# Optimization experiments

Measured on AMD Instinct MI355X. Metric: run time of the kernel, lower is better.

The kernel has to match this reference:

```python
import jax, jax.numpy as jnp
import numpy as np

N_NODES = 50000
N_EDGES = 800000
IN_F, HID_F, OUT_F = 256, 128, 64


def setup_inputs() -> dict:
    key = jax.random.key(0)
    ks = jax.random.split(key, 9)
    glorot = lambda k, shp: jax.random.normal(k, shp, jnp.float32) * np.sqrt(2.0 / (shp[0] + shp[1]))
    return {
        "x": jax.random.normal(ks[0], (N_NODES, IN_F), jnp.float32),
        "W1": glorot(ks[1], (IN_F, HID_F)),
        "b1": jnp.zeros((HID_F,), jnp.float32),
        "W2": glorot(ks[2], (HID_F, OUT_F)),
        "b2": jnp.zeros((OUT_F,), jnp.float32),
        "Wf": glorot(ks[3], (OUT_F, 2)),
        "bf": jnp.zeros((2,), jnp.float32),
        "src": jax.random.randint(ks[4], (N_EDGES,), 0, N_NODES, jnp.int32),
        "dst": jax.random.randint(ks[5], (N_EDGES,), 0, N_NODES, jnp.int32),
    }


def _gcn_layer(x, src, dst, W, b):
    # DGL GraphConv, norm='both': h = D_in^{-1/2} A D_out^{-1/2} (x W) + b
    n = x.shape[0]
    ones = jnp.ones((src.shape[0],), x.dtype)
    deg_out = jnp.clip(jax.ops.segment_sum(ones, src, num_segments=n), 1.0)
    deg_in = jnp.clip(jax.ops.segment_sum(ones, dst, num_segments=n), 1.0)
    h = x @ W  # transform first (in_feats >= out_feats), cheaper messages
    h = h * jax.lax.rsqrt(deg_out)[:, None]
    agg = jax.ops.segment_sum(h[src], dst, num_segments=n)  # [N, F] sparse aggregate
    return agg * jax.lax.rsqrt(deg_in)[:, None] + b


def reference(x, W1, b1, W2, b2, Wf, bf, src, dst):
    h1 = jax.nn.relu(_gcn_layer(x, src, dst, W1, b1))
    hidden = _gcn_layer(h1, src, dst, W2, b2)
    logits = hidden @ Wf + bf
    return (logits, hidden)
```

## Files before the change

### kernel.cpp

```cpp
#include <hip/hip_runtime.h>
#include <hip/hip_bf16.h>
#include <cstdint>
#include <cstddef>

#define NNODES 50000
#define NEDGES 800000
#define DHB    64
#define DHC    12500
#define NCH    256
#define CHUNK1 3125
#define NBUCK  196

typedef unsigned short u16;
typedef unsigned int u32;
typedef short bfrag8 __attribute__((ext_vector_type(8)));
typedef float f32x4 __attribute__((ext_vector_type(4)));

__device__ __forceinline__ u16 f2bf(float f) {
    union { float f; uint32_t i; } v; v.f = f;
    uint32_t r = (v.i + 0x7FFFu + ((v.i >> 16) & 1u)) >> 16;
    return (u16)r;
}
__device__ __forceinline__ float bflo(u32 p) { union { uint32_t i; float f; } v; v.i = p << 16; return v.f; }
__device__ __forceinline__ float bfhi(u32 p) { union { uint32_t i; float f; } v; v.i = p & 0xFFFF0000u; return v.f; }

__global__ __launch_bounds__(256) void pre_kernel(const float* __restrict__ W1, const float* __restrict__ W2,
                                                  u16* __restrict__ P1, u16* __restrict__ P2,
                                                  const int* __restrict__ src, const int* __restrict__ dst,
                                                  u32* __restrict__ histg, u32* __restrict__ gh1, int nE) {
    __shared__ u32 hh[NNODES / 2];
    int b = blockIdx.x, t = threadIdx.x;
    if (b < DHB) {
        for (int j = t; j < NNODES / 2; j += 256) hh[j] = 0;
        __syncthreads();
        int beg = b * DHC, end = min(beg + DHC, nE);
        for (int i = beg + t; i < end; i += 256) {
            u32 n = (u32)src[i];
            atomicAdd(&hh[n >> 1], 1u << ((n & 1) * 16));
        }
        __syncthreads();
        u32* out = histg + (size_t)b * (NNODES / 2);
        for (int j = t; j < NNODES / 2; j += 256) out[j] = hh[j];
    } else if (b < DHB + NCH) {
        int c = b - DHB;
        hh[t] = 0;
        __syncthreads();
        int beg = c * CHUNK1, end = min(beg + CHUNK1, nE);
        for (int i = beg + t; i < end; i += 256)
            atomicAdd(&hh[(u32)dst[i] >> 8], 1);
        __syncthreads();
        gh1[t * NCH + c] = hh[t];
    } else {
        int i = (b - DHB - NCH) * 256 + t;
        if (i < 256 * 128) {
            int k = i >> 7, n = i & 127;
            P1[((((k >> 3) << 7) + n) << 3) | (k & 7)] = f2bf(W1[i]);
        }
        if (i < 128 * 64) {
            int k = i >> 6, n = i & 63;
            P2[((((k >> 3) << 6) + n) << 3) | (k & 7)] = f2bf(W2[i]);
        }
    }
}

__global__ __launch_bounds__(256) void red_scan1(const u32* __restrict__ histg, int* __restrict__ deg,
                                                 const u32* __restrict__ gh1, int* __restrict__ scan1,
                                                 int* __restrict__ part1) {
    int t = threadIdx.x, b = blockIdx.x;
    int n = b * 196 + t;
    if (t < 196 && n < NNODES) {
        int s = 0;
        #pragma unroll 4
        for (int bb = 0; bb < DHB; bb++)
            s += (int)((histg[(size_t)bb * (NNODES / 2) + (n >> 1)] >> ((n & 1) * 16)) & 0xFFFFu);
        deg[n] = s;
    }
    __shared__ int sd[256];
    int gi = b * NCH + t;
    int v = (int)gh1[gi];
    sd[t] = v;
    __syncthreads();
    #pragma unroll
    for (int o = 1; o < 256; o <<= 1) {
        int add = (t >= o) ? sd[t - o] : 0;
        __syncthreads();
        sd[t] += add;
        __syncthreads();
    }
    scan1[gi] = sd[t];
    if (t == 255) part1[b] = sd[255];
}

__global__ __launch_bounds__(256) void scatter1(const int* __restrict__ dst, const int* __restrict__ src,
                                                const u32* __restrict__ gh1, const int* __restrict__ scan1,
                                                const int* __restrict__ part1, u32* __restrict__ sbuf, int nE) {
    __shared__ int sd[256];
    __shared__ int offs[256];
    __shared__ u32 base[256];
    __shared__ u32 lh[256];
    int t = threadIdx.x, c = blockIdx.x;
    int v = part1[t];
    sd[t] = v;
    __syncthreads();
    #pragma unroll
    for (int o = 1; o < 256; o <<= 1) {
        int add = (t >= o) ? sd[t - o] : 0;
        __syncthreads();
        sd[t] += add;
        __syncthreads();
    }
    offs[t] = sd[t] - v;
    __syncthreads();
    base[t] = (u32)(scan1[t * NCH + c] + offs[t] - (int)gh1[t * NCH + c]);
    lh[t] = 0;
    __syncthreads();
    int beg = c * CHUNK1, end = min(beg + CHUNK1, nE);
    for (int i = beg + t; i < end; i += 256) {
        u32 el = ((u32)dst[i] << 16) | (u32)src[i];
        u32 d = el >> 24;
        u32 r = atomicAdd(&lh[d], 1);
        sbuf[base[d] + r] = el;
    }
}

__global__ __launch_bounds__(256) void sort_bucket(const u32* __restrict__ sbuf, const int* __restrict__ part1,
                                                   u32* __restrict__ sorted, int* __restrict__ rp, int nE) {
    __shared__ int sd[256];
    __shared__ int cnt[256];
    __shared__ int cursor[256];
    int t = threadIdx.x, b = blockIdx.x;
    int v = part1[t];
    sd[t] = v;
    __syncthreads();
    #pragma unroll
    for (int o = 1; o < 256; o <<= 1) {
        int add = (t >= o) ? sd[t - o] : 0;
        __syncthreads();
        sd[t] += add;
        __syncthreads();
    }
    __shared__ int bs_s, bl_s;
    if (t == b) { bs_s = sd[t] - v; bl_s = v; }
    __syncthreads();
    int bstart = bs_s, bend = bstart + bl_s;
    cnt[t] = 0;
    __syncthreads();
    for (int i = bstart + t; i < bend; i += 256)
        atomicAdd(&cnt[(sbuf[i] >> 16) & 255u], 1);
    __syncthreads();
    int cv = cnt[t];
    sd[t] = cv;
    __syncthreads();
    #pragma unroll
    for (int o = 1; o < 256; o <<= 1) {
        int add = (t >= o) ? sd[t - o] : 0;
        __syncthreads();
        sd[t] += add;
        __syncthreads();
    }
    int excl = sd[t] - cv;
    int node = b * 256 + t;
    if (node < NNODES) rp[node] = bstart + excl;
    if (b == NBUCK - 1 && t == 0) rp[NNODES] = nE;
    cursor[t] = excl;
    __syncthreads();
    for (int i = bstart + t; i < bend; i += 256) {
        u32 el = sbuf[i];
        int r = atomicAdd(&cursor[(el >> 16) & 255u], 1);
        sorted[bstart + r] = el;
    }
}


template <int K, int N, bool AF32>
__global__ __launch_bounds__(256) void gemm_scaled(const void* __restrict__ A_, const u16* __restrict__ Wp,
                                                   const int* __restrict__ deg, u16* __restrict__ out, int M) {
    const int lane = threadIdx.x & 63;
    const int wave = threadIdx.x >> 6;
    const int m = lane & 15;
    const int q = lane >> 4;
    const int row0 = blockIdx.x * 64 + wave * 16;

    int rowa = row0 + m; if (rowa > M - 1) rowa = M - 1;

    constexpr int NT = N / 16;
    f32x4 acc[NT];
    #pragma unroll
    for (int t = 0; t < NT; t++) acc[t] = (f32x4){0.f, 0.f, 0.f, 0.f};

    #pragma unroll
    for (int kc = 0; kc < K; kc += 32) {
        bfrag8 af;
        if constexpr (AF32) {
            const float* ap = (const float*)A_ + (size_t)rowa * K + q * 8 + kc;
            const float4 x0 = *(const float4*)(ap);
            const float4 x1 = *(const float4*)(ap + 4);
            af[0] = (short)f2bf(x0.x); af[1] = (short)f2bf(x0.y);
            af[2] = (short)f2bf(x0.z); af[3] = (short)f2bf(x0.w);
            af[4] = (short)f2bf(x1.x); af[5] = (short)f2bf(x1.y);
            af[6] = (short)f2bf(x1.z); af[7] = (short)f2bf(x1.w);
        } else {
            const u16* ap = (const u16*)A_ + (size_t)rowa * K + q * 8 + kc;
            af = *(const bfrag8*)ap;
        }
        const u16* bbase = Wp + ((size_t)(((kc >> 3) + q) * N) + m) * 8;
        #pragma unroll
        for (int t = 0; t < NT; t++) {
            bfrag8 bf_ = *(const bfrag8*)(bbase + t * 128);
            acc[t] = __builtin_amdgcn_mfma_f32_16x16x32_bf16(af, bf_, acc[t], 0, 0, 0);
        }
    }
    #pragma unroll
    for (int r = 0; r < 4; r++) {
        int gr = row0 + q * 4 + r;
        if (gr < M) {
            int dO = deg[gr]; if (dO < 1) dO = 1;
            float s = rsqrtf((float)dO);
            #pragma unroll
            for (int t = 0; t < NT; t++)
                out[(size_t)gr * N + t * 16 + m] = f2bf(acc[t][r] * s);
        }
    }
}

__global__ __launch_bounds__(256) void gather1(const uint4* __restrict__ h, const int* __restrict__ row_ptr,
                                               const u32* __restrict__ sorted, const float* __restrict__ b1,
                                               uint4* __restrict__ h1out, int nNodes) {
    int node = (blockIdx.x * 256 + threadIdx.x) >> 4;
    int l = threadIdx.x & 15;
    if (node >= nNodes) return;
    int beg = row_ptr[node], end = row_ptr[node + 1];
    float a[8] = {0.f, 0.f, 0.f, 0.f, 0.f, 0.f, 0.f, 0.f};
    for (int e = beg; e < end; e += 8) {
        uint4 p[8];
        #pragma unroll
        for (int j = 0; j < 8; j++) {
            int ee = e + j; ee = (ee < end - 1) ? ee : end - 1;
            p[j] = h[(size_t)(sorted[ee] & 0xFFFFu) * 16 + l];
        }
        #pragma unroll
        for (int j = 0; j < 8; j++)
            if (e + j < end) {
                a[0] += bflo(p[j].x); a[1] += bfhi(p[j].x);
                a[2] += bflo(p[j].y); a[3] += bfhi(p[j].y);
                a[4] += bflo(p[j].z); a[5] += bfhi(p[j].z);
                a[6] += bflo(p[j].w); a[7] += bfhi(p[j].w);
            }
    }
    int dI = end - beg; if (dI < 1) dI = 1;
    float r = rsqrtf((float)dI);
    const float4 bA = *(const float4*)(b1 + 8 * l);
    const float4 bB = *(const float4*)(b1 + 8 * l + 4);
    float v0 = fmaxf(a[0] * r + bA.x, 0.f), v1 = fmaxf(a[1] * r + bA.y, 0.f);
    float v2 = fmaxf(a[2] * r + bA.z, 0.f), v3 = fmaxf(a[3] * r + bA.w, 0.f);
    float v4 = fmaxf(a[4] * r + bB.x, 0.f), v5 = fmaxf(a[5] * r + bB.y, 0.f);
    float v6 = fmaxf(a[6] * r + bB.z, 0.f), v7 = fmaxf(a[7] * r + bB.w, 0.f);
    uint4 o;
    o.x = ((u32)f2bf(v1) << 16) | f2bf(v0);
    o.y = ((u32)f2bf(v3) << 16) | f2bf(v2);
    o.z = ((u32)f2bf(v5) << 16) | f2bf(v4);
    o.w = ((u32)f2bf(v7) << 16) | f2bf(v6);
    h1out[(size_t)node * 16 + l] = o;
}

__global__ __launch_bounds__(256) void gather2(const uint4* __restrict__ h2, const int* __restrict__ row_ptr,
                                               const u32* __restrict__ sorted, const float* __restrict__ b2,
                                               const float* __restrict__ Wf, const float* __restrict__ bfv,
                                               float* __restrict__ logits, float* __restrict__ hidden, int nNodes) {
    int node = (blockIdx.x * 256 + threadIdx.x) >> 3;
    int l = threadIdx.x & 7;
    if (node >= nNodes) return;
    int beg = row_ptr[node], end = row_ptr[node + 1];
    float a[8] = {0.f, 0.f, 0.f, 0.f, 0.f, 0.f, 0.f, 0.f};
    for (int e = beg; e < end; e += 8) {
        uint4 p[8];
        #pragma unroll
        for (int j = 0; j < 8; j++) {
            int ee = e + j; ee = (ee < end - 1) ? ee : end - 1;
            p[j] = h2[(size_t)(sorted[ee] & 0xFFFFu) * 8 + l];
        }
        #pragma unroll
        for (int j = 0; j < 8; j++)
            if (e + j < end) {
                a[0] += bflo(p[j].x); a[1] += bfhi(p[j].x);
                a[2] += bflo(p[j].y); a[3] += bfhi(p[j].y);
                a[4] += bflo(p[j].z); a[5] += bfhi(p[j].z);
                a[6] += bflo(p[j].w); a[7] += bfhi(p[j].w);
            }
    }
    int dI = end - beg; if (dI < 1) dI = 1;
    float r = rsqrtf((float)dI);
    float v[8];
    #pragma unroll
    for (int f = 0; f < 8; f++) v[f] = a[f] * r + b2[8 * l + f];
    float4 oA = {v[0], v[1], v[2], v[3]};
    float4 oB = {v[4], v[5], v[6], v[7]};
    ((float4*)hidden)[(size_t)node * 16 + 2 * l + 0] = oA;
    ((float4*)hidden)[(size_t)node * 16 + 2 * l + 1] = oB;
    float l0 = 0.f, l1 = 0.f;
    #pragma unroll
    for (int f = 0; f < 8; f++) {
        l0 += v[f] * Wf[(8 * l + f) * 2 + 0];
        l1 += v[f] * Wf[(8 * l + f) * 2 + 1];
    }
    #pragma unroll
    for (int off = 4; off > 0; off >>= 1) {
        l0 += __shfl_down(l0, off, 8);
        l1 += __shfl_down(l1, off, 8);
    }
    if (l == 0) {
        logits[(size_t)node * 2 + 0] = l0 + bfv[0];
        logits[(size_t)node * 2 + 1] = l1 + bfv[1];
    }
}

extern "C" void kernel_launch(void* const* d_in, const int* in_sizes, int n_in,
                              void* d_out, int out_size, void* d_ws, size_t ws_size,
                              hipStream_t stream) {
    const float* x   = (const float*)d_in[0];
    const float* W1  = (const float*)d_in[1];
    const float* b1  = (const float*)d_in[2];
    const float* W2  = (const float*)d_in[3];
    const float* b2  = (const float*)d_in[4];
    const float* Wf  = (const float*)d_in[5];
    const float* bfv = (const float*)d_in[6];
    const int* src = (const int*)d_in[7];
    const int* dst = (const int*)d_in[8];

    float* out_logits = (float*)d_out;
    float* out_hidden = (float*)d_out + 2 * NNODES;

    char* ws = (char*)d_ws;
    size_t off = 0;
    auto alloc = [&](size_t bytes) { void* p = ws + off; off += (bytes + 255) & ~(size_t)255; return p; };
    u32*   gh1     = (u32*)alloc(NCH * NCH * 4);
    int*   scan1   = (int*)alloc(NCH * NCH * 4);
    int*   part1   = (int*)alloc(256 * 4);
    u32*   sbuf    = (u32*)alloc((size_t)NEDGES * 4);
    u32*   sorted  = (u32*)alloc((size_t)NEDGES * 4);
    u32*   histg   = (u32*)alloc((size_t)DHB * (NNODES / 2) * 4);
    int*   deg_out = (int*)alloc(NNODES * 4);
    int*   row_ptr = (int*)alloc((NNODES + 1) * 4);
    u16*   Wp1     = (u16*)alloc(256 * 128 * 2);
    u16*   Wp2     = (u16*)alloc(128 * 64 * 2);
    u16*   h       = (u16*)alloc((size_t)NNODES * 128 * 2);
    u16*   h1      = (u16*)alloc((size_t)NNODES * 128 * 2);
    u16*   h2      = (u16*)alloc((size_t)NNODES * 64 * 2);

    pre_kernel<<<DHB + NCH + 128, 256, 0, stream>>>(W1, W2, Wp1, Wp2, src, dst, histg, gh1, NEDGES);
    red_scan1<<<NCH, 256, 0, stream>>>(histg, deg_out, gh1, scan1, part1);
    scatter1<<<NCH, 256, 0, stream>>>(dst, src, gh1, scan1, part1, sbuf, NEDGES);
    sort_bucket<<<NBUCK, 256, 0, stream>>>(sbuf, part1, sorted, row_ptr, NEDGES);
    gemm_scaled<256, 128, true><<<(NNODES + 63) / 64, 256, 0, stream>>>(x, Wp1, deg_out, h, NNODES);
    gather1<<<(NNODES * 16 + 255) / 256, 256, 0, stream>>>((const uint4*)h, row_ptr, sorted, b1,
                                                           (uint4*)h1, NNODES);
    gemm_scaled<128, 64, false><<<(NNODES + 63) / 64, 256, 0, stream>>>(h1, Wp2, deg_out, h2, NNODES);
    gather2<<<(NNODES * 8 + 255) / 256, 256, 0, stream>>>((const uint4*)h2, row_ptr, sorted, b2, Wf, bfv,
                                                          out_logits, out_hidden, NNODES);
}
```

Before: 217.5 us.

## Use global atomic degrees, fuse sort with first GEMM, degree-sort gather nodes

Per-node degrees are now computed with global atomics in the histogram pass, replacing the per-block shared histograms and the reduction kernel. The bucket sort and the first GEMM run in one launch so independent work overlaps. A counting sort of nodes by in-degree (capped at 63) builds a permutation, and both gathers use it so threads in a wave get similar edge counts, reducing divergence. The cost is global atomic contention on the degree arrays, a memset, and scattered output writes through the permutation.

```diff
diff --git a/kernel.cpp b/kernel.cpp
--- a/kernel.cpp
+++ b/kernel.cpp
@@ -5,11 +5,12 @@
 
 #define NNODES 50000
 #define NEDGES 800000
-#define DHB    64
-#define DHC    12500
 #define NCH    256
 #define CHUNK1 3125
 #define NBUCK  196
+#define GB1    782
+#define DPB    64
+#define NPB    782
 
 typedef unsigned short u16;
 typedef unsigned int u32;
@@ -27,31 +28,24 @@
 __global__ __launch_bounds__(256) void pre_kernel(const float* __restrict__ W1, const float* __restrict__ W2,
                                                   u16* __restrict__ P1, u16* __restrict__ P2,
                                                   const int* __restrict__ src, const int* __restrict__ dst,
-                                                  u32* __restrict__ histg, u32* __restrict__ gh1, int nE) {
-    __shared__ u32 hh[NNODES / 2];
+                                                  int* __restrict__ deg_out, int* __restrict__ deg_in,
+                                                  u32* __restrict__ gh1, int nE) {
     int b = blockIdx.x, t = threadIdx.x;
-    if (b < DHB) {
-        for (int j = t; j < NNODES / 2; j += 256) hh[j] = 0;
-        __syncthreads();
-        int beg = b * DHC, end = min(beg + DHC, nE);
+    if (b < NCH) {
+        __shared__ u32 hh[NCH];
+        hh[t] = 0;
+        __syncthreads();
+        int beg = b * CHUNK1, end = min(beg + CHUNK1, nE);
         for (int i = beg + t; i < end; i += 256) {
-            u32 n = (u32)src[i];
-            atomicAdd(&hh[n >> 1], 1u << ((n & 1) * 16));
-        }
-        __syncthreads();
-        u32* out = histg + (size_t)b * (NNODES / 2);
-        for (int j = t; j < NNODES / 2; j += 256) out[j] = hh[j];
-    } else if (b < DHB + NCH) {
-        int c = b - DHB;
-        hh[t] = 0;
-        __syncthreads();
-        int beg = c * CHUNK1, end = min(beg + CHUNK1, nE);
-        for (int i = beg + t; i < end; i += 256)
-            atomicAdd(&hh[(u32)dst[i] >> 8], 1);
-        __syncthreads();
-        gh1[t * NCH + c] = hh[t];
+            int d = dst[i];
+            atomicAdd(&hh[(u32)d >> 8], 1u);
+            atomicAdd(&deg_in[d], 1);
+            atomicAdd(&deg_out[src[i]], 1);
+        }
+        __syncthreads();
+        gh1[t * NCH + b] = hh[t];
     } else {
-        int i = (b - DHB - NCH) * 256 + t;
+        int i = (b - NCH) * 256 + t;
         if (i < 256 * 128) {
             int k = i >> 7, n = i & 127;
             P1[((((k >> 3) << 7) + n) << 3) | (k & 7)] = f2bf(W1[i]);
@@ -63,42 +57,68 @@
     }
 }
 
-__global__ __launch_bounds__(256) void red_scan1(const u32* __restrict__ histg, int* __restrict__ deg,
-                                                 const u32* __restrict__ gh1, int* __restrict__ scan1,
-                                                 int* __restrict__ part1) {
+__global__ __launch_bounds__(256) void scan_hist(const u32* __restrict__ gh1, int* __restrict__ scan1,
+                                                 int* __restrict__ part1, const int* __restrict__ deg_in,
+                                                 int* __restrict__ gdh) {
     int t = threadIdx.x, b = blockIdx.x;
-    int n = b * 196 + t;
-    if (t < 196 && n < NNODES) {
-        int s = 0;
-        #pragma unroll 4
-        for (int bb = 0; bb < DHB; bb++)
-            s += (int)((histg[(size_t)bb * (NNODES / 2) + (n >> 1)] >> ((n & 1) * 16)) & 0xFFFFu);
-        deg[n] = s;
-    }
-    __shared__ int sd[256];
-    int gi = b * NCH + t;
-    int v = (int)gh1[gi];
-    sd[t] = v;
-    __syncthreads();
-    #pragma unroll
-    for (int o = 1; o < 256; o <<= 1) {
-        int add = (t >= o) ? sd[t - o] : 0;
-        __syncthreads();
-        sd[t] += add;
-        __syncthreads();
-    }
-    scan1[gi] = sd[t];
-    if (t == 255) part1[b] = sd[255];
+    if (b < NCH) {
+        __shared__ int sd[256];
+        int gi = b * NCH + t;
+        int v = (int)gh1[gi];
+        sd[t] = v;
+        __syncthreads();
+        #pragma unroll
+        for (int o = 1; o < 256; o <<= 1) {
+            int add = (t >= o) ? sd[t - o] : 0;
+            __syncthreads();
+            sd[t] += add;
+            __syncthreads();
+        }
+        scan1[gi] = sd[t];
+        if (t == 255) part1[b] = sd[255];
+    } else {
+        int pb = b - NCH;
+        __shared__ int cnt[64];
+        if (t < 64) cnt[t] = 0;
+        __syncthreads();
+        int n0 = pb * NPB, n1 = min(n0 + NPB, NNODES);
+        for (int n = n0 + t; n < n1; n += 256) {
+            int d = deg_in[n]; d = d > 63 ? 63 : d;
+            atomicAdd(&cnt[d], 1);
+        }
+        __syncthreads();
+        if (t < 64) gdh[pb * 64 + t] = cnt[t];
+    }
 }
 
 __global__ __launch_bounds__(256) void scatter1(const int* __restrict__ dst, const int* __restrict__ src,
                                                 const u32* __restrict__ gh1, const int* __restrict__ scan1,
-                                                const int* __restrict__ part1, u32* __restrict__ sbuf, int nE) {
+                                                const int* __restrict__ part1, u32* __restrict__ sbuf,
+                                                const int* __restrict__ gdh, int* __restrict__ gbase, int nE) {
+    int t = threadIdx.x, c = blockIdx.x;
+    if (c == NCH) {
+        __shared__ int colsum[64];
+        if (t < 64) {
+            int s = 0;
+            for (int pb = 0; pb < DPB; pb++) s += gdh[pb * 64 + t];
+            colsum[t] = s;
+        }
+        __syncthreads();
+        if (t == 0) {
+            int s = 0;
+            for (int d = 0; d < 64; d++) { int c0 = colsum[d]; colsum[d] = s; s += c0; }
+        }
+        __syncthreads();
+        if (t < 64) {
+            int s = colsum[t];
+            for (int pb = 0; pb < DPB; pb++) { gbase[pb * 64 + t] = s; s += gdh[pb * 64 + t]; }
+        }
+        return;
+    }
     __shared__ int sd[256];
     __shared__ int offs[256];
     __shared__ u32 base[256];
     __shared__ u32 lh[256];
-    int t = threadIdx.x, c = blockIdx.x;
     int v = part1[t];
     sd[t] = v;
     __syncthreads();
@@ -123,63 +143,14 @@
     }
 }
 
-__global__ __launch_bounds__(256) void sort_bucket(const u32* __restrict__ sbuf, const int* __restrict__ part1,
-                                                   u32* __restrict__ sorted, int* __restrict__ rp, int nE) {
-    __shared__ int sd[256];
-    __shared__ int cnt[256];
-    __shared__ int cursor[256];
-    int t = threadIdx.x, b = blockIdx.x;
-    int v = part1[t];
-    sd[t] = v;
-    __syncthreads();
-    #pragma unroll
-    for (int o = 1; o < 256; o <<= 1) {
-        int add = (t >= o) ? sd[t - o] : 0;
-        __syncthreads();
-        sd[t] += add;
-        __syncthreads();
-    }
-    __shared__ int bs_s, bl_s;
-    if (t == b) { bs_s = sd[t] - v; bl_s = v; }
-    __syncthreads();
-    int bstart = bs_s, bend = bstart + bl_s;
-    cnt[t] = 0;
-    __syncthreads();
-    for (int i = bstart + t; i < bend; i += 256)
-        atomicAdd(&cnt[(sbuf[i] >> 16) & 255u], 1);
-    __syncthreads();
-    int cv = cnt[t];
-    sd[t] = cv;
-    __syncthreads();
-    #pragma unroll
-    for (int o = 1; o < 256; o <<= 1) {
-        int add = (t >= o) ? sd[t - o] : 0;
-        __syncthreads();
-        sd[t] += add;
-        __syncthreads();
-    }
-    int excl = sd[t] - cv;
-    int node = b * 256 + t;
-    if (node < NNODES) rp[node] = bstart + excl;
-    if (b == NBUCK - 1 && t == 0) rp[NNODES] = nE;
-    cursor[t] = excl;
-    __syncthreads();
-    for (int i = bstart + t; i < bend; i += 256) {
-        u32 el = sbuf[i];
-        int r = atomicAdd(&cursor[(el >> 16) & 255u], 1);
-        sorted[bstart + r] = el;
-    }
-}
-
-
 template <int K, int N, bool AF32>
-__global__ __launch_bounds__(256) void gemm_scaled(const void* __restrict__ A_, const u16* __restrict__ Wp,
-                                                   const int* __restrict__ deg, u16* __restrict__ out, int M) {
+__device__ __forceinline__ void gemm_body(const void* __restrict__ A_, const u16* __restrict__ Wp,
+                                          const int* __restrict__ deg, u16* __restrict__ out, int M, int bx) {
     const int lane = threadIdx.x & 63;
     const int wave = threadIdx.x >> 6;
     const int m = lane & 15;
     const int q = lane >> 4;
-    const int row0 = blockIdx.x * 64 + wave * 16;
+    const int row0 = bx * 64 + wave * 16;
 
     int rowa = row0 + m; if (rowa > M - 1) rowa = M - 1;
 
@@ -223,12 +194,87 @@
     }
 }
 
+template <int K, int N, bool AF32>
+__global__ __launch_bounds__(256) void gemm_scaled(const void* __restrict__ A_, const u16* __restrict__ Wp,
+                                                   const int* __restrict__ deg, u16* __restrict__ out, int M) {
+    gemm_body<K, N, AF32>(A_, Wp, deg, out, M, blockIdx.x);
+}
+
+__global__ __launch_bounds__(256) void sort_gemm(const u32* __restrict__ sbuf, const int* __restrict__ part1,
+                                                 u32* __restrict__ sorted, int* __restrict__ rp,
+                                                 const float* __restrict__ x, const u16* __restrict__ Wp1,
+                                                 const int* __restrict__ deg_out, const int* __restrict__ deg_in,
+                                                 const int* __restrict__ gbase, int* __restrict__ perm,
+                                                 u16* __restrict__ h, int nE) {
+    int b = blockIdx.x, t = threadIdx.x;
+    if (b < NBUCK) {
+        __shared__ int sd[256];
+        __shared__ int cnt[256];
+        __shared__ int cursor[256];
+        int v = part1[t];
+        sd[t] = v;
+        __syncthreads();
+        #pragma unroll
+        for (int o = 1; o < 256; o <<= 1) {
+            int add = (t >= o) ? sd[t - o] : 0;
+            __syncthreads();
+            sd[t] += add;
+            __syncthreads();
+        }
+        __shared__ int bs_s, bl_s;
+        if (t == b) { bs_s = sd[t] - v; bl_s = v; }
+        __syncthreads();
+        int bstart = bs_s, bend = bstart + bl_s;
+        cnt[t] = 0;
+        __syncthreads();
+        for (int i = bstart + t; i < bend; i += 256)
+            atomicAdd(&cnt[(sbuf[i] >> 16) & 255u], 1);
+        __syncthreads();
+        int cv = cnt[t];
+        sd[t] = cv;
+        __syncthreads();
+        #pragma unroll
+        for (int o = 1; o < 256; o <<= 1) {
+            int add = (t >= o) ? sd[t - o] : 0;
+            __syncthreads();
+            sd[t] += add;
+            __syncthreads();
+        }
+        int excl = sd[t] - cv;
+        int node = b * 256 + t;
+        if (node < NNODES) rp[node] = bstart + excl;
+        if (b == NBUCK - 1 && t == 0) rp[NNODES] = nE;
+        cursor[t] = excl;
+        __syncthreads();
+        for (int i = bstart + t; i < bend; i += 256) {
+            u32 el = sbuf[i];
+            int r = atomicAdd(&cursor[(el >> 16) & 255u], 1);
+            sorted[bstart + r] = el;
+        }
+    } else if (b < NBUCK + GB1) {
+        gemm_body<256, 128, true>(x, Wp1, deg_out, h, NNODES, b - NBUCK);
+    } else {
+        int pb = b - NBUCK - GB1;
+        __shared__ int cur[64];
+        if (t < 64) cur[t] = gbase[pb * 64 + t];
+        __syncthreads();
+        int n0 = pb * NPB, n1 = min(n0 + NPB, NNODES);
+        for (int n = n0 + t; n < n1; n += 256) {
+            int d = deg_in[n]; d = d > 63 ? 63 : d;
+            int p = atomicAdd(&cur[d], 1);
+            perm[p] = n;
+        }
+    }
+}
+
 __global__ __launch_bounds__(256) void gather1(const uint4* __restrict__ h, const int* __restrict__ row_ptr,
                                                const u32* __restrict__ sorted, const float* __restrict__ b1,
+                                               const int* __restrict__ perm,
                                                uint4* __restrict__ h1out, int nNodes) {
-    int node = (blockIdx.x * 256 + threadIdx.x) >> 4;
+    int g = (blockIdx.x * 256 + threadIdx.x) >> 4;
     int l = threadIdx.x & 15;
-    if (node >= nNodes) return;
+    if (g >= nNodes) return;
+    int node = perm[g];
     int beg = row_ptr[node], end = row_ptr[node + 1];
     float a[8] = {0.f, 0.f, 0.f, 0.f, 0.f, 0.f, 0.f, 0.f};
     for (int e = beg; e < end; e += 8) {
@@ -266,10 +312,12 @@
 __global__ __launch_bounds__(256) void gather2(const uint4* __restrict__ h2, const int* __restrict__ row_ptr,
                                                const u32* __restrict__ sorted, const float* __restrict__ b2,
                                                const float* __restrict__ Wf, const float* __restrict__ bfv,
+                                               const int* __restrict__ perm,
                                                float* __restrict__ logits, float* __restrict__ hidden, int nNodes) {
-    int node = (blockIdx.x * 256 + threadIdx.x) >> 3;
+    int g = (blockIdx.x * 256 + threadIdx.x) >> 3;
     int l = threadIdx.x & 7;
-    if (node >= nNodes) return;
+    if (g >= nNodes) return;
+    int node = perm[g];
     int beg = row_ptr[node], end = row_ptr[node + 1];
     float a[8] = {0.f, 0.f, 0.f, 0.f, 0.f, 0.f, 0.f, 0.f};
     for (int e = beg; e < end; e += 8) {
@@ -338,23 +386,29 @@
     int*   part1   = (int*)alloc(256 * 4);
     u32*   sbuf    = (u32*)alloc((size_t)NEDGES * 4);
     u32*   sorted  = (u32*)alloc((size_t)NEDGES * 4);
-    u32*   histg   = (u32*)alloc((size_t)DHB * (NNODES / 2) * 4);
-    int*   deg_out = (int*)alloc(NNODES * 4);
+    int*   deg     = (int*)alloc(2 * NNODES * 4);
     int*   row_ptr = (int*)alloc((NNODES + 1) * 4);
+    int*   gdh     = (int*)alloc(DPB * 64 * 4);
+    int*   gbase   = (int*)alloc(DPB * 64 * 4);
+    int*   perm    = (int*)alloc(NNODES * 4);
     u16*   Wp1     = (u16*)alloc(256 * 128 * 2);
     u16*   Wp2     = (u16*)alloc(128 * 64 * 2);
     u16*   h       = (u16*)alloc((size_t)NNODES * 128 * 2);
     u16*   h1      = (u16*)alloc((size_t)NNODES * 128 * 2);
     u16*   h2      = (u16*)alloc((size_t)NNODES * 64 * 2);
 
-    pre_kernel<<<DHB + NCH + 128, 256, 0, stream>>>(W1, W2, Wp1, Wp2, src, dst, histg, gh1, NEDGES);
-    red_scan1<<<NCH, 256, 0, stream>>>(histg, deg_out, gh1, scan1, part1);
-    scatter1<<<NCH, 256, 0, stream>>>(dst, src, gh1, scan1, part1, sbuf, NEDGES);
-    sort_bucket<<<NBUCK, 256, 0, stream>>>(sbuf, part1, sorted, row_ptr, NEDGES);
-    gemm_scaled<256, 128, true><<<(NNODES + 63) / 64, 256, 0, stream>>>(x, Wp1, deg_out, h, NNODES);
-    gather1<<<(NNODES * 16 + 255) / 256, 256, 0, stream>>>((const uint4*)h, row_ptr, sorted, b1,
-                                                           (uint4*)h1, NNODES);
-    gemm_scaled<128, 64, false><<<(NNODES + 63) / 64, 256, 0, stream>>>(h1, Wp2, deg_out, h2, NNODES);
+    int* deg_out = deg;
+    int* deg_in  = deg + NNODES;
+
+    hipMemsetAsync(deg, 0, 2 * NNODES * sizeof(int), stream);
+    pre_kernel<<<NCH + 128, 256, 0, stream>>>(W1, W2, Wp1, Wp2, src, dst, deg_out, deg_in, gh1, NEDGES);
+    scan_hist<<<NCH + DPB, 256, 0, stream>>>(gh1, scan1, part1, deg_in, gdh);
+    scatter1<<<NCH + 1, 256, 0, stream>>>(dst, src, gh1, scan1, part1, sbuf, gdh, gbase, NEDGES);
+    sort_gemm<<<NBUCK + GB1 + DPB, 256, 0, stream>>>(sbuf, part1, sorted, row_ptr, x, Wp1,
+                                                     deg_out, deg_in, gbase, perm, h, NEDGES);
+    gather1<<<(NNODES * 16) / 256, 256, 0, stream>>>((const uint4*)h, row_ptr, sorted, b1, perm,
+                                                     (uint4*)h1, NNODES);
+    gemm_scaled<128, 64, false><<<GB1, 256, 0, stream>>>(h1, Wp2, deg_out, h2, NNODES);
     gather2<<<(NNODES * 8 + 255) / 256, 256, 0, stream>>>((const uint4*)h2, row_ptr, sorted, b2, Wf, bfv,
-                                                          out_logits, out_hidden, NNODES);
-}
+                                                          perm, out_logits, out_hidden, NNODES);
+}
```

New measurement: 253.6 us. +16.6%, slower.
